# Optimization experiments

Measured on AMD Instinct MI355X. Metric: run time of the kernel, lower is better.

## Reference

```python
import jax, jax.numpy as jnp
import numpy as np
from jax import lax

NUM_PROPAGATIONS = 20
N_NODES = 100000
N_EDGES = 3200000
F_IN = 512
HIDDEN = 64
N_CLASSES = 64


def setup_inputs() -> dict:
    key = jax.random.key(0)
    ks = jax.random.split(key, 8)
    return {
        "node_features": jax.random.normal(ks[0], (N_NODES, F_IN), dtype=jnp.float32),
        "edge_weights": jax.random.uniform(ks[1], (N_EDGES,), dtype=jnp.float32),
        "W1": jax.random.normal(ks[2], (F_IN, HIDDEN), dtype=jnp.float32) * (1.0 / np.sqrt(F_IN)),
        "b1": jnp.zeros((HIDDEN,), dtype=jnp.float32),
        "W2": jax.random.normal(ks[3], (HIDDEN, N_CLASSES), dtype=jnp.float32) * (1.0 / np.sqrt(HIDDEN)),
        "b2": jnp.zeros((N_CLASSES,), dtype=jnp.float32),
        "Wg": jax.random.normal(ks[4], (N_CLASSES, 1), dtype=jnp.float32) * (1.0 / np.sqrt(N_CLASSES)),
        "bg": jnp.zeros((1,), dtype=jnp.float32),
        "senders": jax.random.randint(ks[5], (N_EDGES,), 0, N_NODES, dtype=jnp.int32),
        "receivers": jax.random.randint(ks[6], (N_EDGES,), 0, N_NODES, dtype=jnp.int32),
    }


def reference(node_features, edge_weights, W1, b1, W2, b2, Wg, bg, senders, receivers):
    n = node_features.shape[0]

    def spmm(x):  # sparse A @ x via gather + segment_sum, [n, c] -> [n, c]
        return jax.ops.segment_sum(edge_weights[:, None] * x[senders], receivers, num_segments=n)

    # MLP head (training=False -> dropout is identity)
    h = jax.nn.relu(node_features @ W1 + b1)          # [n, hidden]
    logits = h @ W2 + b2                              # [n, c]

    def step(carry, _):
        nxt = spmm(carry)
        return nxt, nxt

    _, hops = lax.scan(step, logits, None, length=NUM_PROPAGATIONS)  # [K, n, c]
    stack = jnp.concatenate([logits[:, None, :], jnp.transpose(hops, (1, 0, 2))], axis=1)  # [n, K+1, c]

    # GatedSum: sigmoid(Linear(1)) per hop, weighted sum over hops
    scale = jax.nn.sigmoid(jnp.squeeze(stack @ Wg + bg, axis=-1))    # [n, K+1]
    return jnp.einsum('nkl,nk->nl', stack, scale)                    # [n, c]
```

## Files before the change

### kernel.cpp

```cpp
#include <hip/hip_runtime.h>
#include <math.h>


#define F_IN 512
#define C 64

__device__ inline float h2f(ushort u) {
  _Float16 h; __builtin_memcpy(&h, &u, 2); return (float)h;
}
__device__ inline ushort f2h(float f) {
  _Float16 h = (_Float16)f; ushort u; __builtin_memcpy(&u, &h, 2); return u;
}

__global__ __launch_bounds__(256) void gemm1_relu(
    const float* __restrict__ A, const float* __restrict__ W1,
    const float* __restrict__ b1, float* __restrict__ H, int M)
{
  __shared__ __align__(16) float As[16][68];
  __shared__ __align__(16) float Bs[16][64];
  int t = threadIdx.x;
  int tx = t & 15, ty = t >> 4;
  int m0 = blockIdx.x * 64;
  int lm = t >> 2, lk = (t & 3) << 2;
  const float* Arow = A + (size_t)(m0 + lm) * F_IN;
  bool aok = (m0 + lm) < M;
  float acc[4][4] = {};

  for (int k0 = 0; k0 < F_IN; k0 += 16) {
    float4 av = make_float4(0.f, 0.f, 0.f, 0.f);
    if (aok) av = *(const float4*)(Arow + k0 + lk);
    float bv[4];
#pragma unroll
    for (int i = 0; i < 4; ++i)
      bv[i] = W1[(size_t)(k0 + (t >> 6) + (i << 2)) * C + (t & 63)];
    __syncthreads();
    As[lk + 0][lm] = av.x; As[lk + 1][lm] = av.y;
    As[lk + 2][lm] = av.z; As[lk + 3][lm] = av.w;
#pragma unroll
    for (int i = 0; i < 4; ++i)
      Bs[(t >> 6) + (i << 2)][t & 63] = bv[i];
    __syncthreads();
#pragma unroll
    for (int kk = 0; kk < 16; ++kk) {
      float4 a = *(const float4*)&As[kk][ty << 2];
      float4 b = *(const float4*)&Bs[kk][tx << 2];
      acc[0][0] += a.x * b.x; acc[0][1] += a.x * b.y; acc[0][2] += a.x * b.z; acc[0][3] += a.x * b.w;
      acc[1][0] += a.y * b.x; acc[1][1] += a.y * b.y; acc[1][2] += a.y * b.z; acc[1][3] += a.y * b.w;
      acc[2][0] += a.z * b.x; acc[2][1] += a.z * b.y; acc[2][2] += a.z * b.z; acc[2][3] += a.z * b.w;
      acc[3][0] += a.w * b.x; acc[3][1] += a.w * b.y; acc[3][2] += a.w * b.z; acc[3][3] += a.w * b.w;
    }
    __syncthreads();
  }
  float4 bb = *(const float4*)&b1[tx << 2];
#pragma unroll
  for (int i = 0; i < 4; ++i) {
    int row = m0 + (ty << 2) + i;
    if (row < M) {
      float4 r;
      r.x = fmaxf(acc[i][0] + bb.x, 0.f);
      r.y = fmaxf(acc[i][1] + bb.y, 0.f);
      r.z = fmaxf(acc[i][2] + bb.z, 0.f);
      r.w = fmaxf(acc[i][3] + bb.w, 0.f);
      *(float4*)&H[(size_t)row * C + (tx << 2)] = r;
    }
  }
}

__global__ __launch_bounds__(256) void gemm2_gate(
    const float* __restrict__ h, const float* __restrict__ W2,
    const float* __restrict__ b2, const float* __restrict__ Wg,
    const float* __restrict__ bgp, ushort* __restrict__ x0,
    float* __restrict__ out, int n)
{
  __shared__ float W2s[C * C];
  int t = threadIdx.x;
  for (int i = t; i < C * C; i += blockDim.x) W2s[i] = W2[i];
  __syncthreads();
  int lane = t & 63, wid = t >> 6;
  int wave = blockIdx.x * (blockDim.x >> 6) + wid;
  int nw = gridDim.x * (blockDim.x >> 6);
  float wg = Wg[lane], bgv = bgp[0], b2v = b2[lane];
  for (int node = wave; node < n; node += nw) {
    float hv = h[(size_t)node * C + lane];
    float acc = b2v;
#pragma unroll
    for (int k = 0; k < C; ++k) {
      float hk = __shfl(hv, k, 64);
      acc += hk * W2s[k * C + lane];
    }
    float p = acc * wg;
#pragma unroll
    for (int off = 32; off > 0; off >>= 1) p += __shfl_xor(p, off, 64);
    float g = 1.f / (1.f + expf(-(p + bgv)));
    size_t o = (size_t)node * C + lane;
    x0[o] = f2h(acc);
    out[o] = g * acc;
  }
}

__global__ void zero_int(int* __restrict__ p, int n) {
  int i = blockIdx.x * blockDim.x + threadIdx.x;
  if (i < n) p[i] = 0;
}

__global__ void hist_recv(const int* __restrict__ recv, int* __restrict__ cnt, int E) {
  int i = blockIdx.x * blockDim.x + threadIdx.x;
  if (i < E) atomicAdd(&cnt[recv[i]], 1);
}

__global__ __launch_bounds__(1024) void scan_counts(
    int* __restrict__ cnt_cursor, int* __restrict__ row_start, int n)
{
  __shared__ int wsum[16];
  int t = threadIdx.x, lane = t & 63, wid = t >> 6;
  int carry = 0;
  for (int base = 0; base < n; base += 1024) {
    int idx = base + t;
    int v = (idx < n) ? cnt_cursor[idx] : 0;
    int incl = v;
#pragma unroll
    for (int off = 1; off < 64; off <<= 1) {
      int u = __shfl_up(incl, off, 64);
      if (lane >= off) incl += u;
    }
    if (lane == 63) wsum[wid] = incl;
    __syncthreads();
    if (t < 16) {
      int ws = wsum[t];
#pragma unroll
      for (int off = 1; off < 16; off <<= 1) {
        int u = __shfl_up(ws, off, 16);
        if ((t & 15) >= off) ws += u;
      }
      wsum[t] = ws;
    }
    __syncthreads();
    int woff = (wid > 0) ? wsum[wid - 1] : 0;
    int total = wsum[15];
    int excl = carry + woff + (incl - v);
    if (idx < n) { row_start[idx] = excl; cnt_cursor[idx] = excl; }
    carry += total;
    __syncthreads();
  }
  if (t == 0) row_start[n] = carry;
}

__global__ void scatter_edges(
    const int* __restrict__ send, const int* __restrict__ recv,
    const float* __restrict__ ew, int* __restrict__ cursor,
    int2* __restrict__ csr, int E)
{
  int i = blockIdx.x * blockDim.x + threadIdx.x;
  if (i < E) {
    int r = recv[i];
    int p = atomicAdd(&cursor[r], 1);
    csr[p] = make_int2(send[i], __float_as_int(ew[i]));
  }
}

__global__ __launch_bounds__(256) void spmm_gate(
    const ushort* __restrict__ x, const int* __restrict__ row_start,
    const int2* __restrict__ csr, const float* __restrict__ Wg,
    const float* __restrict__ bgp, ushort* __restrict__ x_next,
    float* __restrict__ out, int n, float s_in)
{
  int t = threadIdx.x;
  int lane = t & 63, wid = t >> 6;
  int wave = blockIdx.x * (blockDim.x >> 6) + wid;
  int nw = gridDim.x * (blockDim.x >> 6);
  float wg = Wg[lane], bgv = bgp[0];

  for (int node = wave; node < n; node += nw) {
    int beg = row_start[node], end = row_start[node + 1];
    float a0 = 0.f, a1 = 0.f, a2 = 0.f, a3 = 0.f;
    float a4 = 0.f, a5 = 0.f, a6 = 0.f, a7 = 0.f;
    for (int base = beg; base < end; base += 64) {
      int2 ev = make_int2(0, 0);
      if (base + lane < end) ev = csr[base + lane];
      int cnt = end - base; if (cnt > 64) cnt = 64;
      int j = 0;
      for (; j + 8 <= cnt; j += 8) {
        int   s0 = __shfl(ev.x, j + 0, 64), s1 = __shfl(ev.x, j + 1, 64);
        int   s2 = __shfl(ev.x, j + 2, 64), s3 = __shfl(ev.x, j + 3, 64);
        int   s4 = __shfl(ev.x, j + 4, 64), s5 = __shfl(ev.x, j + 5, 64);
        int   s6 = __shfl(ev.x, j + 6, 64), s7 = __shfl(ev.x, j + 7, 64);
        float w0 = __int_as_float(__shfl(ev.y, j + 0, 64));
        float w1 = __int_as_float(__shfl(ev.y, j + 1, 64));
        float w2 = __int_as_float(__shfl(ev.y, j + 2, 64));
        float w3 = __int_as_float(__shfl(ev.y, j + 3, 64));
        float w4 = __int_as_float(__shfl(ev.y, j + 4, 64));
        float w5 = __int_as_float(__shfl(ev.y, j + 5, 64));
        float w6 = __int_as_float(__shfl(ev.y, j + 6, 64));
        float w7 = __int_as_float(__shfl(ev.y, j + 7, 64));
        ushort u0 = x[(unsigned)(s0 * C) + lane];
        ushort u1 = x[(unsigned)(s1 * C) + lane];
        ushort u2 = x[(unsigned)(s2 * C) + lane];
        ushort u3 = x[(unsigned)(s3 * C) + lane];
        ushort u4 = x[(unsigned)(s4 * C) + lane];
        ushort u5 = x[(unsigned)(s5 * C) + lane];
        ushort u6 = x[(unsigned)(s6 * C) + lane];
        ushort u7 = x[(unsigned)(s7 * C) + lane];
        a0 += w0 * h2f(u0); a1 += w1 * h2f(u1);
        a2 += w2 * h2f(u2); a3 += w3 * h2f(u3);
        a4 += w4 * h2f(u4); a5 += w5 * h2f(u5);
        a6 += w6 * h2f(u6); a7 += w7 * h2f(u7);
      }
      for (; j < cnt; ++j) {
        int sj = __shfl(ev.x, j, 64);
        float wj = __int_as_float(__shfl(ev.y, j, 64));
        a0 += wj * h2f(x[(unsigned)(sj * C) + lane]);
      }
    }
    float acc = ((a0 + a1) + (a2 + a3)) + ((a4 + a5) + (a6 + a7));
    float p = acc * wg;
#pragma unroll
    for (int off = 32; off > 0; off >>= 1) p += __shfl_xor(p, off, 64);
    float g = 1.f / (1.f + expf(-(p * s_in + bgv)));
    size_t o = (size_t)node * C + lane;
    x_next[o] = f2h(acc * 0.0625f);
    out[o] += g * (acc * s_in);
  }
}

extern "C" void kernel_launch(void* const* d_in, const int* in_sizes, int n_in,
                              void* d_out, int out_size, void* d_ws, size_t ws_size,
                              hipStream_t stream) {
  const float* nf   = (const float*)d_in[0];
  const float* ew   = (const float*)d_in[1];
  const float* W1   = (const float*)d_in[2];
  const float* b1   = (const float*)d_in[3];
  const float* W2   = (const float*)d_in[4];
  const float* b2   = (const float*)d_in[5];
  const float* Wg   = (const float*)d_in[6];
  const float* bg   = (const float*)d_in[7];
  const int* send   = (const int*)d_in[8];
  const int* recv   = (const int*)d_in[9];
  float* out = (float*)d_out;

  int n = in_sizes[0] / F_IN;
  int E = in_sizes[1];

  float*  hbuf = (float*)d_ws;
  ushort* xA   = (ushort*)(hbuf + (size_t)n * C);
  ushort* xB   = xA + (size_t)n * C;
  int2*   csr  = (int2*)(xB + (size_t)n * C);
  int* row_start = (int*)(csr + E);
  int* cursor    = row_start + (n + 1);

  gemm1_relu<<<(n + 63) / 64, 256, 0, stream>>>(nf, W1, b1, hbuf, n);

  gemm2_gate<<<(n + 3) / 4, 256, 0, stream>>>(hbuf, W2, b2, Wg, bg, xA, out, n);

  zero_int<<<(n + 255) / 256, 256, 0, stream>>>(cursor, n);
  hist_recv<<<(E + 255) / 256, 256, 0, stream>>>(recv, cursor, E);
  scan_counts<<<1, 1024, 0, stream>>>(cursor, row_start, n);
  scatter_edges<<<(E + 255) / 256, 256, 0, stream>>>(send, recv, ew, cursor,
                                                     csr, E);

  ushort* xin = xA;
  ushort* xout = xB;
  for (int k = 0; k < 20; ++k) {
    float s_in = ldexpf(1.0f, 4 * k);
    spmm_gate<<<(n + 3) / 4, 256, 0, stream>>>(xin, row_start, csr, Wg, bg,
                                               xout, out, n, s_in);
    ushort* tmp = xin; xin = xout; xout = tmp;
  }
}
```

Baseline: 2.499 ms.

## Store all hop results and apply gating in one final pass

When the workspace is large enough, each propagation hop is written to its own fp16 slot. The per-hop gating and the read-modify-write of the fp32 output are removed from the SpMM loop, and a single gate_sum kernel applies all gates at the end. The SpMM kernel now has each half-wave handle alternate edges with ushort2 loads and combines the halves with a shuffle. This avoids 20 fp32 read-modify-writes of out but adds about 21 slots of workspace and one extra pass over them. A fallback path keeps the old fused kernel for small workspaces.

Result: faster. 2.258 ms (-9.7%).

```diff
diff --git a/kernel.cpp b/kernel.cpp
--- a/kernel.cpp
+++ b/kernel.cpp
@@ -70,7 +70,7 @@
     const float* __restrict__ h, const float* __restrict__ W2,
     const float* __restrict__ b2, const float* __restrict__ Wg,
     const float* __restrict__ bgp, ushort* __restrict__ x0,
-    float* __restrict__ out, int n)
+    float* __restrict__ out, int n, int write_out)
 {
   __shared__ float W2s[C * C];
   int t = threadIdx.x;
@@ -88,13 +88,15 @@
       float hk = __shfl(hv, k, 64);
       acc += hk * W2s[k * C + lane];
     }
-    float p = acc * wg;
-#pragma unroll
-    for (int off = 32; off > 0; off >>= 1) p += __shfl_xor(p, off, 64);
-    float g = 1.f / (1.f + expf(-(p + bgv)));
     size_t o = (size_t)node * C + lane;
     x0[o] = f2h(acc);
-    out[o] = g * acc;
+    if (write_out) {
+      float p = acc * wg;
+#pragma unroll
+      for (int off = 32; off > 0; off >>= 1) p += __shfl_xor(p, off, 64);
+      float g = 1.f / (1.f + expf(-(p + bgv)));
+      out[o] = g * acc;
+    }
   }
 }
 
@@ -158,52 +160,123 @@
   }
 }
 
-__global__ __launch_bounds__(256) void spmm_gate(
+__global__ __launch_bounds__(256) void spmm_pair(
     const ushort* __restrict__ x, const int* __restrict__ row_start,
-    const int2* __restrict__ csr, const float* __restrict__ Wg,
-    const float* __restrict__ bgp, ushort* __restrict__ x_next,
-    float* __restrict__ out, int n, float s_in)
+    const int2* __restrict__ csr, ushort* __restrict__ x_next, int n)
 {
   int t = threadIdx.x;
   int lane = t & 63, wid = t >> 6;
-  int wave = blockIdx.x * (blockDim.x >> 6) + wid;
-  int nw = gridDim.x * (blockDim.x >> 6);
-  float wg = Wg[lane], bgv = bgp[0];
+  int half = lane >> 5;
+  int ch2 = (lane & 31) << 1;
+  int wave = blockIdx.x * 4 + wid;
+  int nw = gridDim.x * 4;
 
   for (int node = wave; node < n; node += nw) {
     int beg = row_start[node], end = row_start[node + 1];
-    float a0 = 0.f, a1 = 0.f, a2 = 0.f, a3 = 0.f;
-    float a4 = 0.f, a5 = 0.f, a6 = 0.f, a7 = 0.f;
+    float ax0 = 0.f, ay0 = 0.f, ax1 = 0.f, ay1 = 0.f;
+    float ax2 = 0.f, ay2 = 0.f, ax3 = 0.f, ay3 = 0.f;
     for (int base = beg; base < end; base += 64) {
       int2 ev = make_int2(0, 0);
       if (base + lane < end) ev = csr[base + lane];
       int cnt = end - base; if (cnt > 64) cnt = 64;
       int j = 0;
       for (; j + 8 <= cnt; j += 8) {
+        int i0 = j + 0 + half, i1 = j + 2 + half;
+        int i2 = j + 4 + half, i3 = j + 6 + half;
+        int   s0 = __shfl(ev.x, i0, 64), s1 = __shfl(ev.x, i1, 64);
+        int   s2 = __shfl(ev.x, i2, 64), s3 = __shfl(ev.x, i3, 64);
+        float w0 = __int_as_float(__shfl(ev.y, i0, 64));
+        float w1 = __int_as_float(__shfl(ev.y, i1, 64));
+        float w2 = __int_as_float(__shfl(ev.y, i2, 64));
+        float w3 = __int_as_float(__shfl(ev.y, i3, 64));
+        ushort2 u0 = *(const ushort2*)&x[(unsigned)(s0 * C) + ch2];
+        ushort2 u1 = *(const ushort2*)&x[(unsigned)(s1 * C) + ch2];
+        ushort2 u2 = *(const ushort2*)&x[(unsigned)(s2 * C) + ch2];
+        ushort2 u3 = *(const ushort2*)&x[(unsigned)(s3 * C) + ch2];
+        ax0 += w0 * h2f(u0.x); ay0 += w0 * h2f(u0.y);
+        ax1 += w1 * h2f(u1.x); ay1 += w1 * h2f(u1.y);
+        ax2 += w2 * h2f(u2.x); ay2 += w2 * h2f(u2.y);
+        ax3 += w3 * h2f(u3.x); ay3 += w3 * h2f(u3.y);
+      }
+      for (; j < cnt; j += 2) {
+        int i0 = j + half;
+        int s0 = __shfl(ev.x, i0, 64);
+        float w0 = __int_as_float(__shfl(ev.y, i0, 64));
+        ushort2 u0 = *(const ushort2*)&x[(unsigned)(s0 * C) + ch2];
+        ax0 += w0 * h2f(u0.x); ay0 += w0 * h2f(u0.y);
+      }
+    }
+    float sx = (ax0 + ax1) + (ax2 + ax3);
+    float sy = (ay0 + ay1) + (ay2 + ay3);
+    sx += __shfl_xor(sx, 32, 64);
+    sy += __shfl_xor(sy, 32, 64);
+    if (half == 0) {
+      ushort2 uv;
+      uv.x = f2h(sx * 0.0625f);
+      uv.y = f2h(sy * 0.0625f);
+      *(ushort2*)&x_next[(size_t)node * C + ch2] = uv;
+    }
+  }
+}
+
+__global__ __launch_bounds__(256) void gate_sum(
+    const ushort* __restrict__ slots, const float* __restrict__ Wg,
+    const float* __restrict__ bgp, float* __restrict__ out,
+    int n, int K1, size_t slotStride)
+{
+  int t = threadIdx.x;
+  int lane = t & 63, wid = t >> 6;
+  int wave = blockIdx.x * 4 + wid;
+  int nw = gridDim.x * 4;
+  float wg = Wg[lane], bgv = bgp[0];
+  for (int node = wave; node < n; node += nw) {
+    float acc = 0.f;
+    float scale = 1.f;
+    size_t o = (size_t)node * C + lane;
+    for (int k = 0; k < K1; ++k) {
+      float v = h2f(slots[(size_t)k * slotStride + o]);
+      float p = v * wg;
+#pragma unroll
+      for (int off = 32; off > 0; off >>= 1) p += __shfl_xor(p, off, 64);
+      float g = 1.f / (1.f + expf(-(p * scale + bgv)));
+      acc += g * (v * scale);
+      scale *= 16.f;
+    }
+    out[o] = acc;
+  }
+}
+
+__global__ __launch_bounds__(256) void spmm_gate(
+    const ushort* __restrict__ x, const int* __restrict__ row_start,
+    const int2* __restrict__ csr, const float* __restrict__ Wg,
+    const float* __restrict__ bgp, ushort* __restrict__ x_next,
+    float* __restrict__ out, int n, float s_in)
+{
+  int t = threadIdx.x;
+  int lane = t & 63, wid = t >> 6;
+  int wave = blockIdx.x * (blockDim.x >> 6) + wid;
+  int nw = gridDim.x * (blockDim.x >> 6);
+  float wg = Wg[lane], bgv = bgp[0];
+
+  for (int node = wave; node < n; node += nw) {
+    int beg = row_start[node], end = row_start[node + 1];
+    float a0 = 0.f, a1 = 0.f, a2 = 0.f, a3 = 0.f;
+    for (int base = beg; base < end; base += 64) {
+      int2 ev = make_int2(0, 0);
+      if (base + lane < end) ev = csr[base + lane];
+      int cnt = end - base; if (cnt > 64) cnt = 64;
+      int j = 0;
+      for (; j + 4 <= cnt; j += 4) {
         int   s0 = __shfl(ev.x, j + 0, 64), s1 = __shfl(ev.x, j + 1, 64);
         int   s2 = __shfl(ev.x, j + 2, 64), s3 = __shfl(ev.x, j + 3, 64);
-        int   s4 = __shfl(ev.x, j + 4, 64), s5 = __shfl(ev.x, j + 5, 64);
-        int   s6 = __shfl(ev.x, j + 6, 64), s7 = __shfl(ev.x, j + 7, 64);
         float w0 = __int_as_float(__shfl(ev.y, j + 0, 64));
         float w1 = __int_as_float(__shfl(ev.y, j + 1, 64));
         float w2 = __int_as_float(__shfl(ev.y, j + 2, 64));
         float w3 = __int_as_float(__shfl(ev.y, j + 3, 64));
-        float w4 = __int_as_float(__shfl(ev.y, j + 4, 64));
-        float w5 = __int_as_float(__shfl(ev.y, j + 5, 64));
-        float w6 = __int_as_float(__shfl(ev.y, j + 6, 64));
-        float w7 = __int_as_float(__shfl(ev.y, j + 7, 64));
-        ushort u0 = x[(unsigned)(s0 * C) + lane];
-        ushort u1 = x[(unsigned)(s1 * C) + lane];
-        ushort u2 = x[(unsigned)(s2 * C) + lane];
-        ushort u3 = x[(unsigned)(s3 * C) + lane];
-        ushort u4 = x[(unsigned)(s4 * C) + lane];
-        ushort u5 = x[(unsigned)(s5 * C) + lane];
-        ushort u6 = x[(unsigned)(s6 * C) + lane];
-        ushort u7 = x[(unsigned)(s7 * C) + lane];
-        a0 += w0 * h2f(u0); a1 += w1 * h2f(u1);
-        a2 += w2 * h2f(u2); a3 += w3 * h2f(u3);
-        a4 += w4 * h2f(u4); a5 += w5 * h2f(u5);
-        a6 += w6 * h2f(u6); a7 += w7 * h2f(u7);
+        a0 += w0 * h2f(x[(unsigned)(s0 * C) + lane]);
+        a1 += w1 * h2f(x[(unsigned)(s1 * C) + lane]);
+        a2 += w2 * h2f(x[(unsigned)(s2 * C) + lane]);
+        a3 += w3 * h2f(x[(unsigned)(s3 * C) + lane]);
       }
       for (; j < cnt; ++j) {
         int sj = __shfl(ev.x, j, 64);
@@ -211,7 +284,7 @@
         a0 += wj * h2f(x[(unsigned)(sj * C) + lane]);
       }
     }
-    float acc = ((a0 + a1) + (a2 + a3)) + ((a4 + a5) + (a6 + a7));
+    float acc = (a0 + a1) + (a2 + a3);
     float p = acc * wg;
 #pragma unroll
     for (int off = 32; off > 0; off >>= 1) p += __shfl_xor(p, off, 64);
@@ -239,30 +312,63 @@
 
   int n = in_sizes[0] / F_IN;
   int E = in_sizes[1];
-
-  float*  hbuf = (float*)d_ws;
-  ushort* xA   = (ushort*)(hbuf + (size_t)n * C);
-  ushort* xB   = xA + (size_t)n * C;
-  int2*   csr  = (int2*)(xB + (size_t)n * C);
-  int* row_start = (int*)(csr + E);
-  int* cursor    = row_start + (n + 1);
-
-  gemm1_relu<<<(n + 63) / 64, 256, 0, stream>>>(nf, W1, b1, hbuf, n);
-
-  gemm2_gate<<<(n + 3) / 4, 256, 0, stream>>>(hbuf, W2, b2, Wg, bg, xA, out, n);
-
-  zero_int<<<(n + 255) / 256, 256, 0, stream>>>(cursor, n);
-  hist_recv<<<(E + 255) / 256, 256, 0, stream>>>(recv, cursor, E);
-  scan_counts<<<1, 1024, 0, stream>>>(cursor, row_start, n);
-  scatter_edges<<<(E + 255) / 256, 256, 0, stream>>>(send, recv, ew, cursor,
-                                                     csr, E);
-
-  ushort* xin = xA;
-  ushort* xout = xB;
-  for (int k = 0; k < 20; ++k) {
-    float s_in = ldexpf(1.0f, 4 * k);
-    spmm_gate<<<(n + 3) / 4, 256, 0, stream>>>(xin, row_start, csr, Wg, bg,
-                                               xout, out, n, s_in);
-    ushort* tmp = xin; xin = xout; xout = tmp;
-  }
-}
+  const int K = 20;
+
+  size_t slotElems = (size_t)n * C;
+  size_t need = slotElems * 4
+              + (size_t)(K + 1) * slotElems * 2
+              + (size_t)E * 8
+              + (size_t)(2 * n + 1) * 4;
+
+  if (ws_size >= need) {
+    float*  hbuf = (float*)d_ws;
+    ushort* slots = (ushort*)(hbuf + slotElems);
+    int2*   csr  = (int2*)(slots + (size_t)(K + 1) * slotElems);
+    int* row_start = (int*)(csr + E);
+    int* cursor    = row_start + (n + 1);
+
+    gemm1_relu<<<(n + 63) / 64, 256, 0, stream>>>(nf, W1, b1, hbuf, n);
+    gemm2_gate<<<(n + 3) / 4, 256, 0, stream>>>(hbuf, W2, b2, Wg, bg,
+                                                slots, out, n, 0);
+
+    zero_int<<<(n + 255) / 256, 256, 0, stream>>>(cursor, n);
+    hist_recv<<<(E + 255) / 256, 256, 0, stream>>>(recv, cursor, E);
+    scan_counts<<<1, 1024, 0, stream>>>(cursor, row_start, n);
+    scatter_edges<<<(E + 255) / 256, 256, 0, stream>>>(send, recv, ew, cursor,
+                                                       csr, E);
+
+    for (int k = 0; k < K; ++k) {
+      spmm_pair<<<(n + 3) / 4, 256, 0, stream>>>(
+          slots + (size_t)k * slotElems, row_start, csr,
+          slots + (size_t)(k + 1) * slotElems, n);
+    }
+    gate_sum<<<(n + 3) / 4, 256, 0, stream>>>(slots, Wg, bg, out, n, K + 1,
+                                              slotElems);
+  } else {
+    float*  hbuf = (float*)d_ws;
+    ushort* xA   = (ushort*)(hbuf + slotElems);
+    ushort* xB   = xA + slotElems;
+    int2*   csr  = (int2*)(xB + slotElems);
+    int* row_start = (int*)(csr + E);
+    int* cursor    = row_start + (n + 1);
+
+    gemm1_relu<<<(n + 63) / 64, 256, 0, stream>>>(nf, W1, b1, hbuf, n);
+    gemm2_gate<<<(n + 3) / 4, 256, 0, stream>>>(hbuf, W2, b2, Wg, bg,
+                                                xA, out, n, 1);
+
+    zero_int<<<(n + 255) / 256, 256, 0, stream>>>(cursor, n);
+    hist_recv<<<(E + 255) / 256, 256, 0, stream>>>(recv, cursor, E);
+    scan_counts<<<1, 1024, 0, stream>>>(cursor, row_start, n);
+    scatter_edges<<<(E + 255) / 256, 256, 0, stream>>>(send, recv, ew, cursor,
+                                                       csr, E);
+
+    ushort* xin = xA;
+    ushort* xout = xB;
+    for (int k = 0; k < K; ++k) {
+      float s_in = ldexpf(1.0f, 4 * k);
+      spmm_gate<<<(n + 3) / 4, 256, 0, stream>>>(xin, row_start, csr, Wg, bg,
+                                                 xout, out, n, s_in);
+      ushort* tmp = xin; xin = xout; xout = tmp;
+    }
+  }
+}
```
